# Optimization experiments

Hardware: AMD Instinct MI355X
Metric: run time of the kernel (lower is better)

Reference implementation:

```python
import jax, jax.numpy as jnp
import numpy as np

N_NODES = 100_000
N_EDGES = 1_600_000
N_GRAPHS = 64
IN_CH = 128
HID = 64
OUT_CH = 2


def setup_inputs() -> dict:
    key = jax.random.key(0)
    ks = jax.random.split(key, 12)

    def lin(k, fan_in, fan_out):
        s = 1.0 / np.sqrt(fan_in)
        return jax.random.uniform(k, (fan_in, fan_out), jnp.float32, -s, s)

    x = jax.random.normal(ks[0], (N_NODES, IN_CH), jnp.float32)
    edge_index = jax.random.randint(ks[1], (2, N_EDGES), 0, N_NODES, jnp.int64)
    batch = jnp.sort(jax.random.randint(ks[2], (N_NODES,), 0, N_GRAPHS, jnp.int64))
    return {
        "x": x,
        "edge_index": edge_index,
        "batch": batch,
        "w_rel0": lin(ks[3], IN_CH, HID),
        "b_rel0": jnp.zeros((HID,), jnp.float32),
        "w_root0": lin(ks[4], IN_CH, HID),
        "w_rel1": lin(ks[5], HID, HID),
        "b_rel1": jnp.zeros((HID,), jnp.float32),
        "w_root1": lin(ks[6], HID, HID),
        "w_rel2": lin(ks[7], HID, HID),
        "b_rel2": jnp.zeros((HID,), jnp.float32),
        "w_root2": lin(ks[8], HID, HID),
        "head_w1": lin(ks[9], HID, HID),
        "head_b1": jnp.zeros((HID,), jnp.float32),
        "head_w2": lin(ks[10], HID, OUT_CH),
        "head_b2": jnp.zeros((OUT_CH,), jnp.float32),
    }


def _graph_conv(x, src, dst, w_rel, b_rel, w_root):
    # PyG GraphConv: out = lin_rel(sum_{j->i} x_j) + lin_root(x_i)
    agg = jax.ops.segment_sum(x[src], dst, num_segments=N_NODES)  # [N, d_in]
    return agg @ w_rel + b_rel + x @ w_root


def reference(x, edge_index, batch, w_rel0, b_rel0, w_root0,
              w_rel1, b_rel1, w_root1, w_rel2, b_rel2, w_root2,
              head_w1, head_b1, head_w2, head_b2):
    src, dst = edge_index[0], edge_index[1]
    h = jax.nn.relu(_graph_conv(x, src, dst, w_rel0, b_rel0, w_root0))
    h = jax.nn.relu(_graph_conv(h, src, dst, w_rel1, b_rel1, w_root1))
    h = jax.nn.relu(_graph_conv(h, src, dst, w_rel2, b_rel2, w_root2))
    # global_mean_pool over graph ids (dropout is identity at inference)
    sums = jax.ops.segment_sum(h, batch, num_segments=N_GRAPHS)          # [G, H]
    cnts = jax.ops.segment_sum(jnp.ones((N_NODES,), h.dtype), batch,
                               num_segments=N_GRAPHS)                    # [G]
    pooled = sums / jnp.maximum(cnts, 1.0)[:, None]
    z = jax.nn.relu(pooled @ head_w1 + head_b1)
    return z @ head_w2 + head_b2
```

## Files before the change

### kernel.cpp

```cpp
#include <hip/hip_runtime.h>
#include <hip/hip_bf16.h>
#include <hip/hip_cooperative_groups.h>

namespace cg = cooperative_groups;

#define CAP 64
#define KBUCK 391
#define BSHIFT 8
#define BCAP 4608
#define CHUNK_A 2048
#define AITER (CHUNK_A / 256)
#define SA0 40
#define LDSZ 32768

typedef __attribute__((ext_vector_type(8))) short short8;
typedef __attribute__((ext_vector_type(4))) float f32x4;
typedef __hip_bfloat16 bf16;

__device__ inline unsigned short bfbits(float f) {
    bf16 b = __float2bfloat16(f);
    unsigned short u;
    __builtin_memcpy(&u, &b, 2);
    return u;
}

__device__ inline void prep_zero_body(int gtid, int tot,
    const float* wr0, const float* wt0, const float* wr1, const float* wt1,
    const float* wr2, const float* wt2, bf16* hi, bf16* lo,
    int* gcur, float* gsum, int* gcnt)
{
    for (int i = gtid; i < KBUCK; i += tot) gcur[i] = 0;
    for (int i = gtid; i < 64 * 64; i += tot) gsum[i] = 0.f;
    for (int i = gtid; i < 64; i += tot) gcnt[i] = 0;
    for (int idx = gtid; idx < 32768; idx += tot) {
        const float *wr, *wt;
        int n, k;
        if (idx < 16384)      { wr = wr0; wt = wt0; int q = idx;         n = q >> 7; k = q & 127; }
        else if (idx < 24576) { wr = wr1; wt = wt1; int q = idx - 16384; n = q >> 6; k = q & 63; }
        else                  { wr = wr2; wt = wt2; int q = idx - 24576; n = q >> 6; k = q & 63; }
        float w = (n < 64) ? wr[k * 64 + n] : wt[k * 64 + (n - 64)];
        bf16 h = __float2bfloat16(w);
        hi[idx] = h;
        lo[idx] = __float2bfloat16(w - __bfloat162float(h));
    }
}

__device__ inline void bucket_body(char* smem, int bb, const int* __restrict__ ei,
                                   int E, int* __restrict__ gcur,
                                   unsigned* __restrict__ bucketed)
{
    int* hist = (int*)smem;
    int* base = hist + KBUCK;
    const int e0 = bb * CHUNK_A;
    const int e1 = min(e0 + CHUNK_A, E);
    for (int i = threadIdx.x; i < KBUCK; i += 256) hist[i] = 0;
    __syncthreads();
    int dreg[AITER];
    #pragma unroll
    for (int it = 0; it < AITER; ++it) {
        int e = e0 + it * 256 + threadIdx.x;
        dreg[it] = (e < e1) ? ei[E + e] : -1;
        if (dreg[it] >= 0) atomicAdd(&hist[dreg[it] >> BSHIFT], 1);
    }
    __syncthreads();
    for (int i = threadIdx.x; i < KBUCK; i += 256) {
        int h = hist[i];
        base[i] = h ? atomicAdd(&gcur[i], h) : 0;
        hist[i] = 0;
    }
    __syncthreads();
    #pragma unroll
    for (int it = 0; it < AITER; ++it) {
        int e = e0 + it * 256 + threadIdx.x;
        if (e < e1) {
            int s = ei[e];
            int d = dreg[it];
            int b = d >> BSHIFT;
            int off = base[b] + atomicAdd(&hist[b], 1);
            if (off < BCAP)
                bucketed[(size_t)b * BCAP + off] = ((unsigned)s << 8) | (unsigned)(d & 255);
        }
    }
}

__device__ inline void build_body(char* smem, int b,
    const unsigned* __restrict__ bucketed, const int* __restrict__ gcur,
    int* __restrict__ cnt, int* __restrict__ slots, int N)
{
    int* lcnt = (int*)smem;
    const int nb0 = b << BSHIFT;
    lcnt[threadIdx.x] = 0;
    __syncthreads();
    const int count = min(gcur[b], BCAP);
    const unsigned* src = bucketed + (size_t)b * BCAP;
    for (int i = threadIdx.x; i < count; i += 256) {
        unsigned p = src[i];
        int dl = (int)(p & 255u);
        int pos = atomicAdd(&lcnt[dl], 1);
        if (pos < CAP) slots[(size_t)(nb0 + dl) * CAP + pos] = (int)(p >> 8);
    }
    __syncthreads();
    int node = nb0 + threadIdx.x;
    if (node < N) cnt[node] = min(lcnt[threadIdx.x], CAP);
}

__device__ inline void lin0_body(char* smem, int bx, const float* __restrict__ x,
    const bf16* __restrict__ whiT, const bf16* __restrict__ wloT,
    const float* __restrict__ b_rel, bf16* __restrict__ y, bf16* __restrict__ r, int N)
{
    bf16* As = (bf16*)smem;
    bf16* Bh = As + 128 * SA0;
    bf16* Bl = Bh + 128 * SA0;
    const int t = threadIdx.x;
    const int lane = t & 63;
    const int wid = t >> 6;
    const int wm = wid >> 1, wn = wid & 1;
    const int node0 = bx * 128;
    const int lrow = lane & 15;
    const int kgrp = lane >> 4;

    f32x4 acc[4][4];
    #pragma unroll
    for (int i = 0; i < 4; ++i)
        #pragma unroll
        for (int j = 0; j < 4; ++j) acc[i][j] = (f32x4){0.f, 0.f, 0.f, 0.f};

    for (int ks = 0; ks < 4; ++ks) {
        #pragma unroll
        for (int p = 0; p < 2; ++p) {
            int c = t + p * 256;
            int m = c >> 2, kc = c & 3;
            int row = node0 + m; if (row >= N) row = N - 1;
            const float* src = x + (size_t)row * 128 + ks * 32 + kc * 8;
            float4 v0 = *(const float4*)src;
            float4 v1 = *(const float4*)(src + 4);
            union { uint4 q; unsigned short s[8]; } pk;
            pk.s[0] = bfbits(v0.x); pk.s[1] = bfbits(v0.y);
            pk.s[2] = bfbits(v0.z); pk.s[3] = bfbits(v0.w);
            pk.s[4] = bfbits(v1.x); pk.s[5] = bfbits(v1.y);
            pk.s[6] = bfbits(v1.z); pk.s[7] = bfbits(v1.w);
            *(uint4*)&As[m * SA0 + kc * 8] = pk.q;
        }
        #pragma unroll
        for (int p = 0; p < 4; ++p) {
            int c = t + p * 256;
            int half = c >> 9;
            int cc = c & 511;
            int n = cc >> 2, kc = cc & 3;
            const bf16* w = half ? wloT : whiT;
            uint4 v = *(const uint4*)(w + (size_t)n * 128 + ks * 32 + kc * 8);
            if (half) *(uint4*)&Bl[n * SA0 + kc * 8] = v;
            else      *(uint4*)&Bh[n * SA0 + kc * 8] = v;
        }
        __syncthreads();

        short8 a[4], bh[4], bl[4];
        #pragma unroll
        for (int i = 0; i < 4; ++i)
            a[i] = *(const short8*)&As[(wm * 64 + i * 16 + lrow) * SA0 + kgrp * 8];
        #pragma unroll
        for (int j = 0; j < 4; ++j) {
            bh[j] = *(const short8*)&Bh[(wn * 64 + j * 16 + lrow) * SA0 + kgrp * 8];
            bl[j] = *(const short8*)&Bl[(wn * 64 + j * 16 + lrow) * SA0 + kgrp * 8];
        }
        #pragma unroll
        for (int i = 0; i < 4; ++i)
            #pragma unroll
            for (int j = 0; j < 4; ++j) {
                acc[i][j] = __builtin_amdgcn_mfma_f32_16x16x32_bf16(a[i], bh[j], acc[i][j], 0, 0, 0);
                acc[i][j] = __builtin_amdgcn_mfma_f32_16x16x32_bf16(a[i], bl[j], acc[i][j], 0, 0, 0);
            }
        __syncthreads();
    }

    #pragma unroll
    for (int i = 0; i < 4; ++i) {
        int mbase = node0 + wm * 64 + i * 16 + kgrp * 4;
        #pragma unroll
        for (int j = 0; j < 4; ++j) {
            int n = wn * 64 + j * 16 + lrow;
            #pragma unroll
            for (int v = 0; v < 4; ++v) {
                int m = mbase + v;
                if (m < N) {
                    float val = acc[i][j][v];
                    if (n < 64) y[(size_t)m * 64 + n] = __float2bfloat16(val);
                    else        r[(size_t)m * 64 + (n - 64)] = __float2bfloat16(val + b_rel[n - 64]);
                }
            }
        }
    }
}

__device__ inline void lin64_body(char* smem, int bx, const bf16* __restrict__ feat,
    const bf16* __restrict__ whiT, const float* __restrict__ b_rel,
    bf16* __restrict__ y, bf16* __restrict__ r, int N)
{
    bf16* As = (bf16*)smem;
    bf16* Bs = As + 128 * SA0;
    const int t = threadIdx.x;
    const int lane = t & 63;
    const int wid = t >> 6;
    const int wm = wid >> 1, wn = wid & 1;
    const int node0 = bx * 128;
    const int lrow = lane & 15;
    const int kgrp = lane >> 4;

    f32x4 acc[4][4];
    #pragma unroll
    for (int i = 0; i < 4; ++i)
        #pragma unroll
        for (int j = 0; j < 4; ++j) acc[i][j] = (f32x4){0.f, 0.f, 0.f, 0.f};

    for (int ks = 0; ks < 2; ++ks) {
        #pragma unroll
        for (int p = 0; p < 2; ++p) {
            int c = t + p * 256;
            int m = c >> 2, kc = c & 3;
            int row = node0 + m; if (row >= N) row = N - 1;
            *(uint4*)&As[m * SA0 + kc * 8] =
                *(const uint4*)(feat + (size_t)row * 64 + ks * 32 + kc * 8);
        }
        #pragma unroll
        for (int p = 0; p < 2; ++p) {
            int c = t + p * 256;
            int n = c >> 2, kc = c & 3;
            *(uint4*)&Bs[n * SA0 + kc * 8] =
                *(const uint4*)(whiT + (size_t)n * 64 + ks * 32 + kc * 8);
        }
        __syncthreads();

        short8 a[4], b[4];
        #pragma unroll
        for (int i = 0; i < 4; ++i)
            a[i] = *(const short8*)&As[(wm * 64 + i * 16 + lrow) * SA0 + kgrp * 8];
        #pragma unroll
        for (int j = 0; j < 4; ++j)
            b[j] = *(const short8*)&Bs[(wn * 64 + j * 16 + lrow) * SA0 + kgrp * 8];
        #pragma unroll
        for (int i = 0; i < 4; ++i)
            #pragma unroll
            for (int j = 0; j < 4; ++j)
                acc[i][j] = __builtin_amdgcn_mfma_f32_16x16x32_bf16(a[i], b[j], acc[i][j], 0, 0, 0);
        __syncthreads();
    }

    #pragma unroll
    for (int i = 0; i < 4; ++i) {
        int mbase = node0 + wm * 64 + i * 16 + kgrp * 4;
        #pragma unroll
        for (int j = 0; j < 4; ++j) {
            int n = wn * 64 + j * 16 + lrow;
            #pragma unroll
            for (int v = 0; v < 4; ++v) {
                int m = mbase + v;
                if (m < N) {
                    float val = acc[i][j][v];
                    if (n < 64) y[(size_t)m * 64 + n] = __float2bfloat16(val);
                    else        r[(size_t)m * 64 + (n - 64)] = __float2bfloat16(val + b_rel[n - 64]);
                }
            }
        }
    }
}

__device__ inline void gather_node(int node, const bf16* __restrict__ y,
    const int* __restrict__ cnt, const int* __restrict__ slots,
    const bf16* __restrict__ rin, bf16* __restrict__ hout)
{
    const int sub = threadIdx.x & 31;
    const int nb = sub >> 3;
    const int ch = (sub & 7) * 8;
    const int deg = cnt[node];
    const int* sl = slots + (size_t)node * CAP;
    const unsigned short* yp = (const unsigned short*)y;

    float a[8], b[8];
    #pragma unroll
    for (int k = 0; k < 8; ++k) { a[k] = 0.f; b[k] = 0.f; }

    #pragma unroll 2
    for (int j = nb; j < deg; j += 8) {
        int n0 = sl[j];
        uint4 v = *(const uint4*)(yp + (size_t)n0 * 64 + ch);
        a[0] += __uint_as_float(v.x << 16); a[1] += __uint_as_float(v.x & 0xffff0000u);
        a[2] += __uint_as_float(v.y << 16); a[3] += __uint_as_float(v.y & 0xffff0000u);
        a[4] += __uint_as_float(v.z << 16); a[5] += __uint_as_float(v.z & 0xffff0000u);
        a[6] += __uint_as_float(v.w << 16); a[7] += __uint_as_float(v.w & 0xffff0000u);
        int j2 = j + 4;
        if (j2 < deg) {
            int n1 = sl[j2];
            uint4 w = *(const uint4*)(yp + (size_t)n1 * 64 + ch);
            b[0] += __uint_as_float(w.x << 16); b[1] += __uint_as_float(w.x & 0xffff0000u);
            b[2] += __uint_as_float(w.y << 16); b[3] += __uint_as_float(w.y & 0xffff0000u);
            b[4] += __uint_as_float(w.z << 16); b[5] += __uint_as_float(w.z & 0xffff0000u);
            b[6] += __uint_as_float(w.w << 16); b[7] += __uint_as_float(w.w & 0xffff0000u);
        }
    }
    #pragma unroll
    for (int k = 0; k < 8; ++k) {
        a[k] += b[k];
        a[k] += __shfl_xor(a[k], 8);
        a[k] += __shfl_xor(a[k], 16);
    }
    if (nb == 0) {
        uint4 rv = *(const uint4*)((const unsigned short*)rin + (size_t)node * 64 + ch);
        float r0 = __uint_as_float(rv.x << 16), r1 = __uint_as_float(rv.x & 0xffff0000u);
        float r2 = __uint_as_float(rv.y << 16), r3 = __uint_as_float(rv.y & 0xffff0000u);
        float r4 = __uint_as_float(rv.z << 16), r5 = __uint_as_float(rv.z & 0xffff0000u);
        float r6 = __uint_as_float(rv.w << 16), r7 = __uint_as_float(rv.w & 0xffff0000u);
        union { uint4 q; unsigned short s[8]; } pk;
        pk.s[0] = bfbits(fmaxf(r0 + a[0], 0.f)); pk.s[1] = bfbits(fmaxf(r1 + a[1], 0.f));
        pk.s[2] = bfbits(fmaxf(r2 + a[2], 0.f)); pk.s[3] = bfbits(fmaxf(r3 + a[3], 0.f));
        pk.s[4] = bfbits(fmaxf(r4 + a[4], 0.f)); pk.s[5] = bfbits(fmaxf(r5 + a[5], 0.f));
        pk.s[6] = bfbits(fmaxf(r6 + a[6], 0.f)); pk.s[7] = bfbits(fmaxf(r7 + a[7], 0.f));
        *(uint4*)((unsigned short*)hout + (size_t)node * 64 + ch) = pk.q;
    }
}

__device__ inline void pool_chunk(int start, int N, const bf16* __restrict__ h,
    const int* __restrict__ batch, float* __restrict__ gsum, int* __restrict__ gcnt)
{
    int lane = threadIdx.x & 63;
    int nb = lane >> 3;
    int ch = (lane & 7) * 8;
    int end = min(start + 64, N);
    const unsigned short* hp = (const unsigned short*)h;

    float a[8];
    #pragma unroll
    for (int k = 0; k < 8; ++k) a[k] = 0.f;
    int runcnt = 0;
    int i = start;
    int gc = batch[start];

    while (i < end) {
        int idx = i + lane; if (idx > end - 1) idx = end - 1;
        int bl = batch[idx];
        unsigned long long diff = __ballot(bl != gc && (i + lane) < end);
        int len = diff ? ((int)__ffsll(diff) - 1) : min(64, end - i);
        for (int j = i + nb; j < i + len; j += 8) {
            uint4 v = *(const uint4*)(hp + (size_t)j * 64 + ch);
            a[0] += __uint_as_float(v.x << 16); a[1] += __uint_as_float(v.x & 0xffff0000u);
            a[2] += __uint_as_float(v.y << 16); a[3] += __uint_as_float(v.y & 0xffff0000u);
            a[4] += __uint_as_float(v.z << 16); a[5] += __uint_as_float(v.z & 0xffff0000u);
            a[6] += __uint_as_float(v.w << 16); a[7] += __uint_as_float(v.w & 0xffff0000u);
        }
        runcnt += len;
        i += len;
        if (diff) {
            #pragma unroll
            for (int k = 0; k < 8; ++k) {
                a[k] += __shfl_xor(a[k], 8);
                a[k] += __shfl_xor(a[k], 16);
                a[k] += __shfl_xor(a[k], 32);
            }
            if (runcnt > 0) {
                if (nb == 0) {
                    #pragma unroll
                    for (int k = 0; k < 8; ++k)
                        atomicAdd(&gsum[gc * 64 + ch + k], a[k]);
                }
                if (lane == 0) atomicAdd(&gcnt[gc], runcnt);
            }
            #pragma unroll
            for (int k = 0; k < 8; ++k) a[k] = 0.f;
            runcnt = 0;
            gc = __shfl(bl, len);
        }
    }
    #pragma unroll
    for (int k = 0; k < 8; ++k) {
        a[k] += __shfl_xor(a[k], 8);
        a[k] += __shfl_xor(a[k], 16);
        a[k] += __shfl_xor(a[k], 32);
    }
    if (runcnt > 0) {
        if (nb == 0) {
            #pragma unroll
            for (int k = 0; k < 8; ++k)
                atomicAdd(&gsum[gc * 64 + ch + k], a[k]);
        }
        if (lane == 0) atomicAdd(&gcnt[gc], runcnt);
    }
}

__device__ inline void head_body(char* smem,
    const float* __restrict__ gsum, const int* __restrict__ gcnt,
    const float* __restrict__ w1, const float* __restrict__ b1,
    const float* __restrict__ w2, const float* __restrict__ b2,
    float* __restrict__ out)
{
    float* pm = (float*)smem;
    float* z  = pm + 64 * 64;
    int t = threadIdx.x;
    for (int i = t; i < 64 * 64; i += 256) {
        int g = i >> 6;
        float cf = (float)gcnt[g];
        if (cf < 1.f) cf = 1.f;
        pm[i] = gsum[i] / cf;
    }
    __syncthreads();
    for (int i = t; i < 64 * 64; i += 256) {
        int g = i >> 6, c = i & 63;
        float a = b1[c];
        #pragma unroll 8
        for (int k = 0; k < 64; ++k) a = fmaf(pm[g * 64 + k], w1[k * 64 + c], a);
        z[i] = fmaxf(a, 0.f);
    }
    __syncthreads();
    for (int i = t; i < 64 * 2; i += 256) {
        int g = i >> 1, o = i & 1;
        float a = b2[o];
        #pragma unroll 8
        for (int k = 0; k < 64; ++k) a = fmaf(z[g * 64 + k], w2[k * 2 + o], a);
        out[i] = a;
    }
}

__global__ __launch_bounds__(256, 4) void mega_kernel(
    const float* x, const int* ei, const int* batch,
    const float* wr0, const float* wt0, const float* wr1, const float* wt1,
    const float* wr2, const float* wt2,
    const float* br0, const float* br1, const float* br2,
    const float* hw1, const float* hb1, const float* hw2, const float* hb2,
    float* out, int N, int E,
    int* cnt, int* slots, unsigned* bucketed, int* gcur,
    bf16* whiT, bf16* wloT, bf16* yA, bf16* rA, bf16* yB, bf16* rB,
    bf16* h0, bf16* h1, float* gsum, int* gcnt)
{
    extern __shared__ char smem[];
    cg::grid_group grid = cg::this_grid();
    const int g = gridDim.x;
    const int tot = g * 256;
    const int gtid = blockIdx.x * 256 + threadIdx.x;
    const int bucket_tiles = (E + CHUNK_A - 1) / CHUNK_A;
    const int gemm_tiles = (N + 127) / 128;
    const int gather_tiles = (N + 7) / 8;
    const int pool_tiles = (((N + 63) / 64) + 3) / 4;

    prep_zero_body(gtid, tot, wr0, wt0, wr1, wt1, wr2, wt2, whiT, wloT, gcur, gsum, gcnt);
    grid.sync();

    for (int t = blockIdx.x; t < bucket_tiles + gemm_tiles; t += g) {
        if (t < bucket_tiles) bucket_body(smem, t, ei, E, gcur, bucketed);
        else                  lin0_body(smem, t - bucket_tiles, x, whiT, wloT, br0, yA, rA, N);
        __syncthreads();
    }
    grid.sync();

    for (int t = blockIdx.x; t < KBUCK; t += g) {
        build_body(smem, t, bucketed, gcur, cnt, slots, N);
        __syncthreads();
    }
    grid.sync();

    for (int t = blockIdx.x; t < gather_tiles; t += g) {
        int node = t * 8 + (threadIdx.x >> 5);
        if (node < N) gather_node(node, yA, cnt, slots, rA, h0);
    }
    grid.sync();

    for (int t = blockIdx.x; t < gemm_tiles; t += g) {
        lin64_body(smem, t, h0, whiT + 16384, br1, yB, rB, N);
        __syncthreads();
    }
    grid.sync();

    for (int t = blockIdx.x; t < gather_tiles; t += g) {
        int node = t * 8 + (threadIdx.x >> 5);
        if (node < N) gather_node(node, yB, cnt, slots, rB, h1);
    }
    grid.sync();

    for (int t = blockIdx.x; t < gemm_tiles; t += g) {
        lin64_body(smem, t, h1, whiT + 24576, br2, yA, rA, N);
        __syncthreads();
    }
    grid.sync();

    for (int t = blockIdx.x; t < gather_tiles; t += g) {
        int node = t * 8 + (threadIdx.x >> 5);
        if (node < N) gather_node(node, yA, cnt, slots, rA, h0);
    }
    grid.sync();

    for (int t = blockIdx.x; t < pool_tiles; t += g) {
        int start = (t * 4 + (threadIdx.x >> 6)) * 64;
        if (start < N) pool_chunk(start, N, h0, batch, gsum, gcnt);
    }
    __threadfence();
    grid.sync();

    if (blockIdx.x == 0)
        head_body(smem, gsum, gcnt, hw1, hb1, hw2, hb2, out);
}

__global__ __launch_bounds__(256) void k_prep(
    const float* wr0, const float* wt0, const float* wr1, const float* wt1,
    const float* wr2, const float* wt2, bf16* hi, bf16* lo,
    int* gcur, float* gsum, int* gcnt)
{
    prep_zero_body(blockIdx.x * 256 + threadIdx.x, gridDim.x * 256,
                   wr0, wt0, wr1, wt1, wr2, wt2, hi, lo, gcur, gsum, gcnt);
}
__global__ __launch_bounds__(256) void k_bucket(const int* ei, int E, int* gcur, unsigned* bucketed)
{
    extern __shared__ char smem[];
    bucket_body(smem, blockIdx.x, ei, E, gcur, bucketed);
}
__global__ __launch_bounds__(256) void k_build(const unsigned* bucketed, const int* gcur,
                                               int* cnt, int* slots, int N)
{
    extern __shared__ char smem[];
    build_body(smem, blockIdx.x, bucketed, gcur, cnt, slots, N);
}
__global__ __launch_bounds__(256) void k_lin0(const float* x, const bf16* whiT, const bf16* wloT,
                                              const float* br, bf16* y, bf16* r, int N)
{
    extern __shared__ char smem[];
    lin0_body(smem, blockIdx.x, x, whiT, wloT, br, y, r, N);
}
__global__ __launch_bounds__(256) void k_lin64(const bf16* feat, const bf16* whiT,
                                               const float* br, bf16* y, bf16* r, int N)
{
    extern __shared__ char smem[];
    lin64_body(smem, blockIdx.x, feat, whiT, br, y, r, N);
}
__global__ __launch_bounds__(256) void k_gather(const bf16* y, const int* cnt, const int* slots,
                                                const bf16* rin, bf16* hout, int N)
{
    int node = blockIdx.x * 8 + (threadIdx.x >> 5);
    if (node < N) gather_node(node, y, cnt, slots, rin, hout);
}
__global__ __launch_bounds__(256) void k_pool(const bf16* h, const int* batch,
                                              float* gsum, int* gcnt, int N)
{
    int start = (blockIdx.x * 4 + (threadIdx.x >> 6)) * 64;
    if (start < N) pool_chunk(start, N, h, batch, gsum, gcnt);
}
__global__ __launch_bounds__(256) void k_head(const float* gsum, const int* gcnt,
    const float* w1, const float* b1, const float* w2, const float* b2, float* out)
{
    extern __shared__ char smem[];
    head_body(smem, gsum, gcnt, w1, b1, w2, b2, out);
}

extern "C" void kernel_launch(void* const* d_in, const int* in_sizes, int n_in,
                              void* d_out, int out_size, void* d_ws, size_t ws_size,
                              hipStream_t stream)
{
    const float* x    = (const float*)d_in[0];
    const int*   ei   = (const int*)d_in[1];
    const int*   batch= (const int*)d_in[2];
    const float* wr0  = (const float*)d_in[3];
    const float* br0  = (const float*)d_in[4];
    const float* wt0  = (const float*)d_in[5];
    const float* wr1  = (const float*)d_in[6];
    const float* br1  = (const float*)d_in[7];
    const float* wt1  = (const float*)d_in[8];
    const float* wr2  = (const float*)d_in[9];
    const float* br2  = (const float*)d_in[10];
    const float* wt2  = (const float*)d_in[11];
    const float* hw1  = (const float*)d_in[12];
    const float* hb1  = (const float*)d_in[13];
    const float* hw2  = (const float*)d_in[14];
    const float* hb2  = (const float*)d_in[15];
    float* out = (float*)d_out;

    int N = in_sizes[0] / 128;
    int E = in_sizes[1] / 2;

    size_t off = 0;
    auto alloc = [&](size_t bytes) -> void* {
        void* p = (char*)d_ws + off;
        off += (bytes + 255) & ~(size_t)255;
        return p;
    };
    int*      cnt      = (int*)alloc((size_t)N * 4);
    int*      slots    = (int*)alloc((size_t)N * CAP * 4);
    unsigned* bucketed = (unsigned*)alloc((size_t)KBUCK * BCAP * 4);
    int*      gcur     = (int*)alloc((size_t)KBUCK * 4);
    bf16* whiT = (bf16*)alloc(32768 * 2);
    bf16* wloT = (bf16*)alloc(32768 * 2);
    bf16* yA   = (bf16*)alloc((size_t)N * 64 * 2);
    bf16* rA   = (bf16*)alloc((size_t)N * 64 * 2);
    bf16* yB   = (bf16*)alloc((size_t)N * 64 * 2);
    bf16* rB   = (bf16*)alloc((size_t)N * 64 * 2);
    bf16* h0   = (bf16*)alloc((size_t)N * 64 * 2);
    bf16* h1   = (bf16*)alloc((size_t)N * 64 * 2);
    float* gsum = (float*)alloc((size_t)64 * 64 * 4);
    int*   gcnt = (int*)alloc((size_t)64 * 4);
    (void)ws_size; (void)n_in;

    const int gemm_blocks   = (N + 127) / 128;
    const int bucket_blocks = (E + CHUNK_A - 1) / CHUNK_A;
    const int gather_blocks = (N + 7) / 8;
    const int pool_blocks   = (((N + 63) / 64) + 3) / 4;

    int coop = 0;
    hipDeviceGetAttribute(&coop, hipDeviceAttributeCooperativeLaunch, 0);
    int occ = 0;
    hipOccupancyMaxActiveBlocksPerMultiprocessor(&occ, mega_kernel, 256, (size_t)LDSZ);

    if (coop && occ >= 1) {
        int grid = occ * 256;
        if (grid > 1024) grid = 1024;
        void* args[] = {
            (void*)&x, (void*)&ei, (void*)&batch,
            (void*)&wr0, (void*)&wt0, (void*)&wr1, (void*)&wt1, (void*)&wr2, (void*)&wt2,
            (void*)&br0, (void*)&br1, (void*)&br2,
            (void*)&hw1, (void*)&hb1, (void*)&hw2, (void*)&hb2,
            (void*)&out, (void*)&N, (void*)&E,
            (void*)&cnt, (void*)&slots, (void*)&bucketed, (void*)&gcur,
            (void*)&whiT, (void*)&wloT, (void*)&yA, (void*)&rA, (void*)&yB, (void*)&rB,
            (void*)&h0, (void*)&h1, (void*)&gsum, (void*)&gcnt };
        hipLaunchCooperativeKernel((void*)mega_kernel, dim3(grid), dim3(256),
                                   args, LDSZ, stream);
    } else {
        k_prep<<<128, 256, 0, stream>>>(wr0, wt0, wr1, wt1, wr2, wt2, whiT, wloT,
                                        gcur, gsum, gcnt);
        k_bucket<<<bucket_blocks, 256, 2 * KBUCK * 4, stream>>>(ei, E, gcur, bucketed);
        k_lin0<<<gemm_blocks, 256, 3 * 128 * SA0 * 2, stream>>>(x, whiT, wloT, br0, yA, rA, N);
        k_build<<<KBUCK, 256, 1024, stream>>>(bucketed, gcur, cnt, slots, N);
        k_gather<<<gather_blocks, 256, 0, stream>>>(yA, cnt, slots, rA, h0, N);
        k_lin64<<<gemm_blocks, 256, 2 * 128 * SA0 * 2, stream>>>(h0, whiT + 16384, br1, yB, rB, N);
        k_gather<<<gather_blocks, 256, 0, stream>>>(yB, cnt, slots, rB, h1, N);
        k_lin64<<<gemm_blocks, 256, 2 * 128 * SA0 * 2, stream>>>(h1, whiT + 24576, br2, yA, rA, N);
        k_gather<<<gather_blocks, 256, 0, stream>>>(yA, cnt, slots, rA, h0, N);
        k_pool<<<pool_blocks, 256, 0, stream>>>(h0, batch, gsum, gcnt, N);
        k_head<<<1, 256, LDSZ, stream>>>(gsum, gcnt, hw1, hb1, hw2, hb2, out);
    }
}
```

Before: 462.2 us.

## Replace cooperative mega-kernel with separate launches and fused pool-head tail

```diff
diff --git a/kernel.cpp b/kernel.cpp
--- a/kernel.cpp
+++ b/kernel.cpp
@@ -1,8 +1,5 @@
 #include <hip/hip_runtime.h>
 #include <hip/hip_bf16.h>
-#include <hip/hip_cooperative_groups.h>
-
-namespace cg = cooperative_groups;
 
 #define CAP 64
 #define KBUCK 391
@@ -11,7 +8,6 @@
 #define CHUNK_A 2048
 #define AITER (CHUNK_A / 256)
 #define SA0 40
-#define LDSZ 32768
 
 typedef __attribute__((ext_vector_type(8))) short short8;
 typedef __attribute__((ext_vector_type(4))) float f32x4;
@@ -24,14 +20,20 @@
     return u;
 }
 
-__device__ inline void prep_zero_body(int gtid, int tot,
-    const float* wr0, const float* wt0, const float* wr1, const float* wt1,
-    const float* wr2, const float* wt2, bf16* hi, bf16* lo,
-    int* gcur, float* gsum, int* gcnt)
-{
+__global__ __launch_bounds__(256) void prep_kernel(
+    const float* __restrict__ wr0, const float* __restrict__ wt0,
+    const float* __restrict__ wr1, const float* __restrict__ wt1,
+    const float* __restrict__ wr2, const float* __restrict__ wt2,
+    bf16* __restrict__ hi, bf16* __restrict__ lo,
+    int* __restrict__ gcur, float* __restrict__ gsum,
+    int* __restrict__ gcnt, int* __restrict__ done)
+{
+    int gtid = blockIdx.x * 256 + threadIdx.x;
+    int tot = gridDim.x * 256;
     for (int i = gtid; i < KBUCK; i += tot) gcur[i] = 0;
     for (int i = gtid; i < 64 * 64; i += tot) gsum[i] = 0.f;
     for (int i = gtid; i < 64; i += tot) gcnt[i] = 0;
+    if (gtid == 0) *done = 0;
     for (int idx = gtid; idx < 32768; idx += tot) {
         const float *wr, *wt;
         int n, k;
@@ -81,27 +83,6 @@
                 bucketed[(size_t)b * BCAP + off] = ((unsigned)s << 8) | (unsigned)(d & 255);
         }
     }
-}
-
-__device__ inline void build_body(char* smem, int b,
-    const unsigned* __restrict__ bucketed, const int* __restrict__ gcur,
-    int* __restrict__ cnt, int* __restrict__ slots, int N)
-{
-    int* lcnt = (int*)smem;
-    const int nb0 = b << BSHIFT;
-    lcnt[threadIdx.x] = 0;
-    __syncthreads();
-    const int count = min(gcur[b], BCAP);
-    const unsigned* src = bucketed + (size_t)b * BCAP;
-    for (int i = threadIdx.x; i < count; i += 256) {
-        unsigned p = src[i];
-        int dl = (int)(p & 255u);
-        int pos = atomicAdd(&lcnt[dl], 1);
-        if (pos < CAP) slots[(size_t)(nb0 + dl) * CAP + pos] = (int)(p >> 8);
-    }
-    __syncthreads();
-    int node = nb0 + threadIdx.x;
-    if (node < N) cnt[node] = min(lcnt[threadIdx.x], CAP);
 }
 
 __device__ inline void lin0_body(char* smem, int bx, const float* __restrict__ x,
@@ -192,17 +173,55 @@
     }
 }
 
-__device__ inline void lin64_body(char* smem, int bx, const bf16* __restrict__ feat,
-    const bf16* __restrict__ whiT, const float* __restrict__ b_rel,
+__global__ __launch_bounds__(256) void fused_l0_kernel(
+    const float* __restrict__ x,
+    const bf16* __restrict__ whiT, const bf16* __restrict__ wloT,
+    const float* __restrict__ b_rel,
+    bf16* __restrict__ y, bf16* __restrict__ r, int N,
+    const int* __restrict__ ei, int E,
+    int* __restrict__ gcur, unsigned* __restrict__ bucketed)
+{
+    extern __shared__ char smem[];
+    int half = blockIdx.x >> 1;
+    if (blockIdx.x & 1) bucket_body(smem, half, ei, E, gcur, bucketed);
+    else                lin0_body(smem, half, x, whiT, wloT, b_rel, y, r, N);
+}
+
+__global__ __launch_bounds__(256) void build_slots_kernel(
+    const unsigned* __restrict__ bucketed, const int* __restrict__ gcur,
+    int* __restrict__ cnt, int* __restrict__ slots, int N)
+{
+    __shared__ int lcnt[256];
+    const int b = blockIdx.x;
+    const int nb0 = b << BSHIFT;
+    lcnt[threadIdx.x] = 0;
+    __syncthreads();
+    const int count = min(gcur[b], BCAP);
+    const unsigned* src = bucketed + (size_t)b * BCAP;
+    for (int i = threadIdx.x; i < count; i += 256) {
+        unsigned p = src[i];
+        int dl = (int)(p & 255u);
+        int pos = atomicAdd(&lcnt[dl], 1);
+        if (pos < CAP) slots[(size_t)(nb0 + dl) * CAP + pos] = (int)(p >> 8);
+    }
+    __syncthreads();
+    int node = nb0 + threadIdx.x;
+    if (node < N) cnt[node] = min(lcnt[threadIdx.x], CAP);
+}
+
+__global__ __launch_bounds__(256) void lin64_kernel(
+    const bf16* __restrict__ feat, const bf16* __restrict__ whiT,
+    const float* __restrict__ b_rel,
     bf16* __restrict__ y, bf16* __restrict__ r, int N)
 {
+    extern __shared__ char smem[];
     bf16* As = (bf16*)smem;
     bf16* Bs = As + 128 * SA0;
     const int t = threadIdx.x;
     const int lane = t & 63;
     const int wid = t >> 6;
     const int wm = wid >> 1, wn = wid & 1;
-    const int node0 = bx * 128;
+    const int node0 = blockIdx.x * 128;
     const int lrow = lane & 15;
     const int kgrp = lane >> 4;
 
@@ -264,10 +283,13 @@
     }
 }
 
-__device__ inline void gather_node(int node, const bf16* __restrict__ y,
-    const int* __restrict__ cnt, const int* __restrict__ slots,
-    const bf16* __restrict__ rin, bf16* __restrict__ hout)
-{
+__global__ __launch_bounds__(256) void gather_relu_kernel(
+    const bf16* __restrict__ y, const int* __restrict__ cnt,
+    const int* __restrict__ slots, const bf16* __restrict__ rin,
+    bf16* __restrict__ hout, int N)
+{
+    const int node = blockIdx.x * 8 + (threadIdx.x >> 5);
+    if (node >= N) return;
     const int sub = threadIdx.x & 31;
     const int nb = sub >> 3;
     const int ch = (sub & 7) * 8;
@@ -385,20 +407,34 @@
     }
 }
 
-__device__ inline void head_body(char* smem,
-    const float* __restrict__ gsum, const int* __restrict__ gcnt,
+__global__ __launch_bounds__(256) void pool_head_kernel(
+    const bf16* __restrict__ h, const int* __restrict__ batch,
+    float* __restrict__ gsum, int* __restrict__ gcnt, int* __restrict__ done,
     const float* __restrict__ w1, const float* __restrict__ b1,
     const float* __restrict__ w2, const float* __restrict__ b2,
-    float* __restrict__ out)
-{
+    float* __restrict__ out, int N)
+{
+    extern __shared__ char smem[];
+    __shared__ int amlast;
+    int start = (blockIdx.x * 4 + (threadIdx.x >> 6)) * 64;
+    if (start < N) pool_chunk(start, N, h, batch, gsum, gcnt);
+    __syncthreads();
+    if (threadIdx.x == 0) {
+        __threadfence();
+        int prev = atomicAdd(done, 1);
+        amlast = (prev == (int)gridDim.x - 1);
+    }
+    __syncthreads();
+    if (!amlast) return;
+
     float* pm = (float*)smem;
     float* z  = pm + 64 * 64;
     int t = threadIdx.x;
     for (int i = t; i < 64 * 64; i += 256) {
         int g = i >> 6;
-        float cf = (float)gcnt[g];
+        float cf = (float)atomicAdd(&gcnt[g], 0);
         if (cf < 1.f) cf = 1.f;
-        pm[i] = gsum[i] / cf;
+        pm[i] = atomicAdd(&gsum[i], 0.f) / cf;
     }
     __syncthreads();
     for (int i = t; i < 64 * 64; i += 256) {
@@ -416,134 +452,6 @@
         for (int k = 0; k < 64; ++k) a = fmaf(z[g * 64 + k], w2[k * 2 + o], a);
         out[i] = a;
     }
-}
-
-__global__ __launch_bounds__(256, 4) void mega_kernel(
-    const float* x, const int* ei, const int* batch,
-    const float* wr0, const float* wt0, const float* wr1, const float* wt1,
-    const float* wr2, const float* wt2,
-    const float* br0, const float* br1, const float* br2,
-    const float* hw1, const float* hb1, const float* hw2, const float* hb2,
-    float* out, int N, int E,
-    int* cnt, int* slots, unsigned* bucketed, int* gcur,
-    bf16* whiT, bf16* wloT, bf16* yA, bf16* rA, bf16* yB, bf16* rB,
-    bf16* h0, bf16* h1, float* gsum, int* gcnt)
-{
-    extern __shared__ char smem[];
-    cg::grid_group grid = cg::this_grid();
-    const int g = gridDim.x;
-    const int tot = g * 256;
-    const int gtid = blockIdx.x * 256 + threadIdx.x;
-    const int bucket_tiles = (E + CHUNK_A - 1) / CHUNK_A;
-    const int gemm_tiles = (N + 127) / 128;
-    const int gather_tiles = (N + 7) / 8;
-    const int pool_tiles = (((N + 63) / 64) + 3) / 4;
-
-    prep_zero_body(gtid, tot, wr0, wt0, wr1, wt1, wr2, wt2, whiT, wloT, gcur, gsum, gcnt);
-    grid.sync();
-
-    for (int t = blockIdx.x; t < bucket_tiles + gemm_tiles; t += g) {
-        if (t < bucket_tiles) bucket_body(smem, t, ei, E, gcur, bucketed);
-        else                  lin0_body(smem, t - bucket_tiles, x, whiT, wloT, br0, yA, rA, N);
-        __syncthreads();
-    }
-    grid.sync();
-
-    for (int t = blockIdx.x; t < KBUCK; t += g) {
-        build_body(smem, t, bucketed, gcur, cnt, slots, N);
-        __syncthreads();
-    }
-    grid.sync();
-
-    for (int t = blockIdx.x; t < gather_tiles; t += g) {
-        int node = t * 8 + (threadIdx.x >> 5);
-        if (node < N) gather_node(node, yA, cnt, slots, rA, h0);
-    }
-    grid.sync();
-
-    for (int t = blockIdx.x; t < gemm_tiles; t += g) {
-        lin64_body(smem, t, h0, whiT + 16384, br1, yB, rB, N);
-        __syncthreads();
-    }
-    grid.sync();
-
-    for (int t = blockIdx.x; t < gather_tiles; t += g) {
-        int node = t * 8 + (threadIdx.x >> 5);
-        if (node < N) gather_node(node, yB, cnt, slots, rB, h1);
-    }
-    grid.sync();
-
-    for (int t = blockIdx.x; t < gemm_tiles; t += g) {
-        lin64_body(smem, t, h1, whiT + 24576, br2, yA, rA, N);
-        __syncthreads();
-    }
-    grid.sync();
-
-    for (int t = blockIdx.x; t < gather_tiles; t += g) {
-        int node = t * 8 + (threadIdx.x >> 5);
-        if (node < N) gather_node(node, yA, cnt, slots, rA, h0);
-    }
-    grid.sync();
-
-    for (int t = blockIdx.x; t < pool_tiles; t += g) {
-        int start = (t * 4 + (threadIdx.x >> 6)) * 64;
-        if (start < N) pool_chunk(start, N, h0, batch, gsum, gcnt);
-    }
-    __threadfence();
-    grid.sync();
-
-    if (blockIdx.x == 0)
-        head_body(smem, gsum, gcnt, hw1, hb1, hw2, hb2, out);
-}
-
-__global__ __launch_bounds__(256) void k_prep(
-    const float* wr0, const float* wt0, const float* wr1, const float* wt1,
-    const float* wr2, const float* wt2, bf16* hi, bf16* lo,
-    int* gcur, float* gsum, int* gcnt)
-{
-    prep_zero_body(blockIdx.x * 256 + threadIdx.x, gridDim.x * 256,
-                   wr0, wt0, wr1, wt1, wr2, wt2, hi, lo, gcur, gsum, gcnt);
-}
-__global__ __launch_bounds__(256) void k_bucket(const int* ei, int E, int* gcur, unsigned* bucketed)
-{
-    extern __shared__ char smem[];
-    bucket_body(smem, blockIdx.x, ei, E, gcur, bucketed);
-}
-__global__ __launch_bounds__(256) void k_build(const unsigned* bucketed, const int* gcur,
-                                               int* cnt, int* slots, int N)
-{
-    extern __shared__ char smem[];
-    build_body(smem, blockIdx.x, bucketed, gcur, cnt, slots, N);
-}
-__global__ __launch_bounds__(256) void k_lin0(const float* x, const bf16* whiT, const bf16* wloT,
-                                              const float* br, bf16* y, bf16* r, int N)
-{
-    extern __shared__ char smem[];
-    lin0_body(smem, blockIdx.x, x, whiT, wloT, br, y, r, N);
-}
-__global__ __launch_bounds__(256) void k_lin64(const bf16* feat, const bf16* whiT,
-                                               const float* br, bf16* y, bf16* r, int N)
-{
-    extern __shared__ char smem[];
-    lin64_body(smem, blockIdx.x, feat, whiT, br, y, r, N);
-}
-__global__ __launch_bounds__(256) void k_gather(const bf16* y, const int* cnt, const int* slots,
-                                                const bf16* rin, bf16* hout, int N)
-{
-    int node = blockIdx.x * 8 + (threadIdx.x >> 5);
-    if (node < N) gather_node(node, y, cnt, slots, rin, hout);
-}
-__global__ __launch_bounds__(256) void k_pool(const bf16* h, const int* batch,
-                                              float* gsum, int* gcnt, int N)
-{
-    int start = (blockIdx.x * 4 + (threadIdx.x >> 6)) * 64;
-    if (start < N) pool_chunk(start, N, h, batch, gsum, gcnt);
-}
-__global__ __launch_bounds__(256) void k_head(const float* gsum, const int* gcnt,
-    const float* w1, const float* b1, const float* w2, const float* b2, float* out)
-{
-    extern __shared__ char smem[];
-    head_body(smem, gsum, gcnt, w1, b1, w2, b2, out);
 }
 
 extern "C" void kernel_launch(void* const* d_in, const int* in_sizes, int n_in,
@@ -591,44 +499,27 @@
     bf16* h1   = (bf16*)alloc((size_t)N * 64 * 2);
     float* gsum = (float*)alloc((size_t)64 * 64 * 4);
     int*   gcnt = (int*)alloc((size_t)64 * 4);
+    int*   done = (int*)alloc(256);
     (void)ws_size; (void)n_in;
 
     const int gemm_blocks   = (N + 127) / 128;
     const int bucket_blocks = (E + CHUNK_A - 1) / CHUNK_A;
     const int gather_blocks = (N + 7) / 8;
     const int pool_blocks   = (((N + 63) / 64) + 3) / 4;
-
-    int coop = 0;
-    hipDeviceGetAttribute(&coop, hipDeviceAttributeCooperativeLaunch, 0);
-    int occ = 0;
-    hipOccupancyMaxActiveBlocksPerMultiprocessor(&occ, mega_kernel, 256, (size_t)LDSZ);
-
-    if (coop && occ >= 1) {
-        int grid = occ * 256;
-        if (grid > 1024) grid = 1024;
-        void* args[] = {
-            (void*)&x, (void*)&ei, (void*)&batch,
-            (void*)&wr0, (void*)&wt0, (void*)&wr1, (void*)&wt1, (void*)&wr2, (void*)&wt2,
-            (void*)&br0, (void*)&br1, (void*)&br2,
-            (void*)&hw1, (void*)&hb1, (void*)&hw2, (void*)&hb2,
-            (void*)&out, (void*)&N, (void*)&E,
-            (void*)&cnt, (void*)&slots, (void*)&bucketed, (void*)&gcur,
-            (void*)&whiT, (void*)&wloT, (void*)&yA, (void*)&rA, (void*)&yB, (void*)&rB,
-            (void*)&h0, (void*)&h1, (void*)&gsum, (void*)&gcnt };
-        hipLaunchCooperativeKernel((void*)mega_kernel, dim3(grid), dim3(256),
-                                   args, LDSZ, stream);
-    } else {
-        k_prep<<<128, 256, 0, stream>>>(wr0, wt0, wr1, wt1, wr2, wt2, whiT, wloT,
-                                        gcur, gsum, gcnt);
-        k_bucket<<<bucket_blocks, 256, 2 * KBUCK * 4, stream>>>(ei, E, gcur, bucketed);
-        k_lin0<<<gemm_blocks, 256, 3 * 128 * SA0 * 2, stream>>>(x, whiT, wloT, br0, yA, rA, N);
-        k_build<<<KBUCK, 256, 1024, stream>>>(bucketed, gcur, cnt, slots, N);
-        k_gather<<<gather_blocks, 256, 0, stream>>>(yA, cnt, slots, rA, h0, N);
-        k_lin64<<<gemm_blocks, 256, 2 * 128 * SA0 * 2, stream>>>(h0, whiT + 16384, br1, yB, rB, N);
-        k_gather<<<gather_blocks, 256, 0, stream>>>(yB, cnt, slots, rB, h1, N);
-        k_lin64<<<gemm_blocks, 256, 2 * 128 * SA0 * 2, stream>>>(h1, whiT + 24576, br2, yA, rA, N);
-        k_gather<<<gather_blocks, 256, 0, stream>>>(yA, cnt, slots, rA, h0, N);
-        k_pool<<<pool_blocks, 256, 0, stream>>>(h0, batch, gsum, gcnt, N);
-        k_head<<<1, 256, LDSZ, stream>>>(gsum, gcnt, hw1, hb1, hw2, hb2, out);
-    }
-}
+    const size_t LDS_L0  = (size_t)3 * 128 * SA0 * 2;
+    const size_t LDS_L64 = (size_t)2 * 128 * SA0 * 2;
+    const size_t LDS_PH  = (size_t)2 * 64 * 64 * 4;
+
+    prep_kernel<<<128, 256, 0, stream>>>(wr0, wt0, wr1, wt1, wr2, wt2,
+                                         whiT, wloT, gcur, gsum, gcnt, done);
+    fused_l0_kernel<<<bucket_blocks + gemm_blocks, 256, LDS_L0, stream>>>(
+        x, whiT, wloT, br0, yA, rA, N, ei, E, gcur, bucketed);
+    build_slots_kernel<<<KBUCK, 256, 0, stream>>>(bucketed, gcur, cnt, slots, N);
+    gather_relu_kernel<<<gather_blocks, 256, 0, stream>>>(yA, cnt, slots, rA, h0, N);
+    lin64_kernel<<<gemm_blocks, 256, LDS_L64, stream>>>(h0, whiT + 16384, br1, yB, rB, N);
+    gather_relu_kernel<<<gather_blocks, 256, 0, stream>>>(yB, cnt, slots, rB, h1, N);
+    lin64_kernel<<<gemm_blocks, 256, LDS_L64, stream>>>(h1, whiT + 24576, br2, yA, rA, N);
+    gather_relu_kernel<<<gather_blocks, 256, 0, stream>>>(yA, cnt, slots, rA, h0, N);
+    pool_head_kernel<<<pool_blocks, 256, LDS_PH, stream>>>(
+        h0, batch, gsum, gcnt, done, hw1, hb1, hw2, hb2, out, N);
+}
```

After: 391.8 us. -15.2%, faster.
